# Performance work log

Hardware: AMD Instinct MI355X
Metric: run time of the kernel (lower is better)

The kernel has to match this reference:

```python
import jax, jax.numpy as jnp
import numpy as np

V = 128          # vocab_size
S = 32           # sentence_size
E = 16           # embedding_size
M = 128          # memory_size
L = 128          # linear_output_size
B = 16
N = 127


def _position_encoding(sentence_size, embedding_size):
    enc = np.ones((embedding_size, sentence_size), dtype=np.float32)
    ls = sentence_size + 1
    le = embedding_size + 1
    for i in range(1, le):
        for j in range(1, ls):
            enc[i - 1, j - 1] = (i - (le - 1) / 2) * (j - (ls - 1) / 2)
    enc = 1 + 4 * enc / embedding_size / sentence_size
    return enc.T  # [S, E]


def setup_inputs() -> dict:
    key = jax.random.key(0)
    ks = jax.random.split(key, 12)
    node_fts = jax.random.randint(ks[0], (B, N, S), 0, V).astype(jnp.float32)
    edge_fts = jax.random.randint(ks[1], (B, N, N, S), 0, V).astype(jnp.float32)
    graph_fts = jax.random.randint(ks[2], (B, S), 0, V).astype(jnp.float32)
    adj_mat = jax.random.randint(ks[3], (B, N, N), 0, 2).astype(jnp.float32)
    hidden = jnp.zeros((B, N, E), jnp.float32)
    sc = 0.02
    query_biases = sc * jax.random.normal(ks[4], (V - 1, E), jnp.float32)
    stories_biases = sc * jax.random.normal(ks[5], (V - 1, E), jnp.float32)
    output_biases = sc * jax.random.normal(ks[6], (V - 1, E), jnp.float32)
    memory_contents = sc * jax.random.normal(ks[7], (M, E), jnp.float32)
    W_int = sc * jax.random.normal(ks[8], (E, E), jnp.float32)   # intermediate_linear (unused, num_hops=1)
    W_out = sc * jax.random.normal(ks[9], (E, L), jnp.float32)   # output_linear
    W_fin = sc * jax.random.normal(ks[10], (L, V), jnp.float32)  # final_linear
    enc = jnp.asarray(_position_encoding(S, E))
    return dict(node_fts=node_fts, edge_fts=edge_fts, graph_fts=graph_fts,
                adj_mat=adj_mat, hidden=hidden, enc=enc,
                query_biases=query_biases, stories_biases=stories_biases,
                output_biases=output_biases, memory_contents=memory_contents,
                W_int=W_int, W_out=W_out, W_fin=W_fin)


def reference(node_fts, edge_fts, graph_fts, adj_mat, hidden, enc,
              query_biases, stories_biases, output_biases, memory_contents,
              W_int, W_out, W_fin):
    del hidden
    b, n, s = node_fts.shape
    # [B, N+1, S]: nodes plus graph feature row
    naf = jnp.concatenate([node_fts, graph_fts[:, None, :]], axis=1)
    # mask edges then pad to [B, N+1, N+1, S]
    ef = edge_fts * adj_mat[..., None]
    ef = jnp.pad(ef, ((0, 0), (0, 1), (0, 1), (0, 0)))
    bt = b * (n + 1)
    queries = naf.reshape(bt, s)                 # [BT, S]
    stories = ef.reshape(bt, n + 1, s)           # [BT, M0, S], M0 = N+1

    nil = jnp.zeros((1, enc.shape[1]), queries.dtype)
    sb = jnp.concatenate([stories_biases, nil], axis=0)   # [V, E]
    qb = jnp.concatenate([query_biases, nil], axis=0)
    ob = jnp.concatenate([output_biases, nil], axis=0)

    sidx = jnp.maximum(stories.astype(jnp.int32), 0)       # clamp_min(0)
    qidx = jnp.maximum(queries.astype(jnp.int32), 0)

    # position-encoded weighted sums over the sentence axis
    mem = jnp.einsum('bmse,se->bme', sb[sidx], enc)        # [BT, M0, E]
    Cj = jnp.einsum('bmse,se->bme', ob[sidx], enc)         # [BT, M0, E]
    pad_m = memory_contents.shape[0] - (n + 1)
    mem = jnp.pad(mem, ((0, 0), (0, pad_m), (0, 0))) + memory_contents
    Cj = jnp.pad(Cj, ((0, 0), (0, pad_m), (0, 0)))
    u = jnp.einsum('bse,se->be', qb[qidx], enc)            # [BT, E]

    # num_hops = 1
    x = u
    probs = jax.nn.softmax(jnp.einsum('bme,be->bm', mem, x), axis=-1)
    o = jnp.einsum('bme,bm->be', Cj, probs)
    x = jax.nn.relu((x + o) @ W_out)                       # last hop -> output_linear + relu
    ret = x @ W_fin                                        # [BT, V]

    nxt = ret.reshape(b, n + 1, -1)
    return nxt[:, :-1, :] + nxt[:, -1:, :]                 # [B, N, V]
```

## Files before the change

kernel.cpp:

```cpp
#include <hip/hip_runtime.h>

#define Vn 128
#define Sn 32
#define En 16
#define M0 128
#define Ln 128
#define Bn 16
#define Nn 127
#define NROWS (Bn * Nn)
#define RS 20

__global__ __launch_bounds__(256, 8) void memnet_fused(
    const float* __restrict__ node_fts, const float* __restrict__ edge_fts,
    const float* __restrict__ graph_fts, const float* __restrict__ adjm,
    const float* __restrict__ enc, const float* __restrict__ qb,
    const float* __restrict__ sb, const float* __restrict__ ob,
    const float* __restrict__ mc, const float* __restrict__ wout,
    const float* __restrict__ wfin, float* __restrict__ out)
{
    __shared__ __align__(16) float sbL[M0 * RS];
    __shared__ __align__(16) float encL[Sn * En];
    __shared__ unsigned int idxw[M0 * 8];
    __shared__ float scoresL[M0];
    __shared__ float probsL[M0];
    __shared__ float uL[En];
    __shared__ float ugL[En];
    __shared__ float uoL[En];
    __shared__ float cM[En];
    __shared__ float cC[En];
    __shared__ float xL[Ln];
    __shared__ float xgL[Ln];
    __shared__ float xg2L[Vn];
    __shared__ float owaveL[4 * En];
    __shared__ float red[4], red2[4];
    __shared__ int listL[128];
    __shared__ int flagL[128];
    __shared__ int wcnt[2];

    const int t = threadIdx.x;
    const int bt = blockIdx.x;
    const int b = bt / 127;
    const int lane = t & 63;
    const int wv = t >> 6;

    for (int c = t; c < 512; c += 256) {
        int r = c >> 2, q = c & 3;
        float4 v = make_float4(0.f, 0.f, 0.f, 0.f);
        if (r < 127) v = *(const float4*)&sb[r * 16 + q * 4];
        *(float4*)&sbL[r * RS + q * 4] = v;
    }
    if (t < 128) *(float4*)&encL[t * 4] = *(const float4*)&enc[t * 4];

    if (t < 128) {
        bool flag = (t < 127) && (adjm[(size_t)bt * 127 + t] != 0.f);
        unsigned long long msk = __ballot(flag);
        int pos = (int)__popcll(msk & ((1ull << lane) - 1ull));
        if (flag) listL[(t & 64) + pos] = t;
        if (lane == 0) wcnt[t >> 6] = (int)__popcll(msk);
        flagL[t] = flag ? 1 : 0;
    }
    for (int c = t; c < 1024; c += 256) {
        int m = c >> 3, q = c & 7;
        if (m < 127 && adjm[(size_t)bt * 127 + m] != 0.f) {
            float4 v = *(const float4*)&edge_fts[(size_t)(bt * 127 + m) * 32 + q * 4];
            idxw[m * 8 + q] = (unsigned)(int)v.x | ((unsigned)(int)v.y << 8)
                            | ((unsigned)(int)v.z << 16) | ((unsigned)(int)v.w << 24);
        }
    }
    if (lane < 16) {
        if (wv == 0) {
            float ue = 0.f;
            for (int s = 0; s < 32; s++) {
                int qi = (int)node_fts[(size_t)bt * 32 + s];
                if (qi < 0) qi = 0;
                float w = (qi < 127) ? qb[qi * 16 + lane] : 0.f;
                ue = fmaf(w, enc[s * 16 + lane], ue);
            }
            uL[lane] = ue;
        } else if (wv == 2) {
            float ue = 0.f;
            for (int s = 0; s < 32; s++) {
                int qi = (int)graph_fts[b * 32 + s];
                if (qi < 0) qi = 0;
                float w = (qi < 127) ? qb[qi * 16 + lane] : 0.f;
                ue = fmaf(w, enc[s * 16 + lane], ue);
            }
            ugL[lane] = ue;
        } else if (wv == 1) {
            float es = 0.f;
            for (int s = 0; s < 32; s++) es += enc[s * 16 + lane];
            cM[lane] = sb[lane] * es;
            cC[lane] = ob[lane] * es;
        }
    }
    __syncthreads();

    if (t < 128 && !flagL[t]) {
        float p = 0.f;
#pragma unroll
        for (int e4 = 0; e4 < 16; e4 += 4) {
            float4 m4 = *(const float4*)&mc[t * 16 + e4];
            p = fmaf(cM[e4 + 0] + m4.x, uL[e4 + 0], p);
            p = fmaf(cM[e4 + 1] + m4.y, uL[e4 + 1], p);
            p = fmaf(cM[e4 + 2] + m4.z, uL[e4 + 2], p);
            p = fmaf(cM[e4 + 3] + m4.w, uL[e4 + 3], p);
        }
        scoresL[t] = p;
    }

    const int eg4 = (t & 3) * 4;
    const int qd = t >> 2;
    const int c0 = wcnt[0];
    const int nact = c0 + wcnt[1];
    const float4 u4 = *(const float4*)&uL[eg4];

    float4 aC_A = make_float4(0.f, 0.f, 0.f, 0.f);
    float4 aC_B = make_float4(0.f, 0.f, 0.f, 0.f);
    int mA = -1, mB = -1;

    if (qd < nact) {
        mA = listL[(qd < c0) ? qd : (qd - c0 + 64)];
        float4 aM = make_float4(0.f, 0.f, 0.f, 0.f);
        for (int sq = 0; sq < 8; sq++) {
            unsigned w0 = idxw[mA * 8 + sq];
#pragma unroll
            for (int j = 0; j < 4; j++) {
                int s = sq * 4 + j;
                int i0 = (w0 >> (8 * j)) & 0xFF;
                int i0c = (i0 < 127) ? i0 : 126;
                float4 eb = *(const float4*)&encL[s * 16 + eg4];
                float4 a0 = *(const float4*)&sbL[i0 * RS + eg4];
                float4 cv = *(const float4*)&ob[i0c * 16 + eg4];
                if (i0 == 127) cv = make_float4(0.f, 0.f, 0.f, 0.f);
                aM.x = fmaf(a0.x, eb.x, aM.x); aM.y = fmaf(a0.y, eb.y, aM.y);
                aM.z = fmaf(a0.z, eb.z, aM.z); aM.w = fmaf(a0.w, eb.w, aM.w);
                aC_A.x = fmaf(cv.x, eb.x, aC_A.x); aC_A.y = fmaf(cv.y, eb.y, aC_A.y);
                aC_A.z = fmaf(cv.z, eb.z, aC_A.z); aC_A.w = fmaf(cv.w, eb.w, aC_A.w);
            }
        }
        float4 mc4 = *(const float4*)&mc[mA * 16 + eg4];
        float p = (aM.x + mc4.x) * u4.x + (aM.y + mc4.y) * u4.y
                + (aM.z + mc4.z) * u4.z + (aM.w + mc4.w) * u4.w;
        p += __shfl_xor(p, 1); p += __shfl_xor(p, 2);
        if ((t & 3) == 0) scoresL[mA] = p;
    }
    if (qd + 64 < nact) {
        int g = qd + 64;
        mB = listL[(g < c0) ? g : (g - c0 + 64)];
        float4 aM = make_float4(0.f, 0.f, 0.f, 0.f);
        for (int sq = 0; sq < 8; sq++) {
            unsigned w0 = idxw[mB * 8 + sq];
#pragma unroll
            for (int j = 0; j < 4; j++) {
                int s = sq * 4 + j;
                int i0 = (w0 >> (8 * j)) & 0xFF;
                int i0c = (i0 < 127) ? i0 : 126;
                float4 eb = *(const float4*)&encL[s * 16 + eg4];
                float4 a0 = *(const float4*)&sbL[i0 * RS + eg4];
                float4 cv = *(const float4*)&ob[i0c * 16 + eg4];
                if (i0 == 127) cv = make_float4(0.f, 0.f, 0.f, 0.f);
                aM.x = fmaf(a0.x, eb.x, aM.x); aM.y = fmaf(a0.y, eb.y, aM.y);
                aM.z = fmaf(a0.z, eb.z, aM.z); aM.w = fmaf(a0.w, eb.w, aM.w);
                aC_B.x = fmaf(cv.x, eb.x, aC_B.x); aC_B.y = fmaf(cv.y, eb.y, aC_B.y);
                aC_B.z = fmaf(cv.z, eb.z, aC_B.z); aC_B.w = fmaf(cv.w, eb.w, aC_B.w);
            }
        }
        float4 mc4 = *(const float4*)&mc[mB * 16 + eg4];
        float p = (aM.x + mc4.x) * u4.x + (aM.y + mc4.y) * u4.y
                + (aM.z + mc4.z) * u4.z + (aM.w + mc4.w) * u4.w;
        p += __shfl_xor(p, 1); p += __shfl_xor(p, 2);
        if ((t & 3) == 0) scoresL[mB] = p;
    }
    __syncthreads();

    float pmask;
    {
        float v = (t < 128) ? scoresL[t] : -1e30f;
#pragma unroll
        for (int off = 32; off > 0; off >>= 1) v = fmaxf(v, __shfl_xor(v, off));
        if (lane == 0) red[wv] = v;
        __syncthreads();
        float mx = fmaxf(fmaxf(red[0], red[1]), fmaxf(red[2], red[3]));
        float ex = (t < 128) ? __expf(scoresL[t] - mx) : 0.f;
        float exm = (t < 128 && !flagL[t]) ? ex : 0.f;
        float sv = ex, sm = exm;
#pragma unroll
        for (int off = 32; off > 0; off >>= 1) {
            sv += __shfl_xor(sv, off);
            sm += __shfl_xor(sm, off);
        }
        __syncthreads();
        if (lane == 0) { red[wv] = sv; red2[wv] = sm; }
        __syncthreads();
        float sum = red[0] + red[1] + red[2] + red[3];
        pmask = (red2[0] + red2[1] + red2[2] + red2[3]) / sum;
        if (t < 128) probsL[t] = ex / sum;
    }
    __syncthreads();

    {
        float4 op = make_float4(0.f, 0.f, 0.f, 0.f);
        if (mA >= 0) {
            float pa = probsL[mA];
            op.x = pa * aC_A.x; op.y = pa * aC_A.y;
            op.z = pa * aC_A.z; op.w = pa * aC_A.w;
        }
        if (mB >= 0) {
            float pb = probsL[mB];
            op.x = fmaf(pb, aC_B.x, op.x); op.y = fmaf(pb, aC_B.y, op.y);
            op.z = fmaf(pb, aC_B.z, op.z); op.w = fmaf(pb, aC_B.w, op.w);
        }
#pragma unroll
        for (int off = 4; off <= 32; off <<= 1) {
            op.x += __shfl_xor(op.x, off);
            op.y += __shfl_xor(op.y, off);
            op.z += __shfl_xor(op.z, off);
            op.w += __shfl_xor(op.w, off);
        }
        if (lane < 4) *(float4*)&owaveL[wv * 16 + lane * 4] = op;
    }
    __syncthreads();
    if (t < 16) {
        float o = owaveL[t] + owaveL[16 + t] + owaveL[32 + t] + owaveL[48 + t];
        uoL[t] = uL[t] + o + cC[t] * pmask;
    }
    __syncthreads();

    if (t < 128) {
        float acc = 0.f;
#pragma unroll
        for (int e = 0; e < 16; e++) acc = fmaf(uoL[e], wout[e * 128 + t], acc);
        xL[t] = fmaxf(acc, 0.f);
    } else {
        int l = t - 128;
        float acc = 0.f;
#pragma unroll
        for (int e = 0; e < 16; e++) acc = fmaf(ugL[e] + cC[e], wout[e * 128 + l], acc);
        xgL[l] = fmaxf(acc, 0.f);
    }
    __syncthreads();

    {
        const int vcol = t & 127;
        const float* xsrc = (t < 128) ? xL : xgL;
        float acc = 0.f;
        for (int l = 0; l < 128; l++) acc = fmaf(xsrc[l], wfin[l * 128 + vcol], acc);
        if (t >= 128) xg2L[vcol] = acc;
        __syncthreads();
        if (t < 128) out[(size_t)bt * 128 + vcol] = acc + xg2L[vcol];
    }
}

extern "C" void kernel_launch(void* const* d_in, const int* in_sizes, int n_in,
                              void* d_out, int out_size, void* d_ws, size_t ws_size,
                              hipStream_t stream)
{
    const float* node  = (const float*)d_in[0];
    const float* edge  = (const float*)d_in[1];
    const float* graph = (const float*)d_in[2];
    const float* adjm  = (const float*)d_in[3];
    const float* enc   = (const float*)d_in[5];
    const float* qb    = (const float*)d_in[6];
    const float* sb    = (const float*)d_in[7];
    const float* ob    = (const float*)d_in[8];
    const float* mc    = (const float*)d_in[9];
    const float* wout  = (const float*)d_in[11];
    const float* wfin  = (const float*)d_in[12];

    memnet_fused<<<NROWS, 256, 0, stream>>>(node, edge, graph, adjm, enc, qb,
                                            sb, ob, mc, wout, wfin, (float*)d_out);
}
```

Baseline: 132.3 us.

## Split output projection into a separate batched tail kernel sharing weights

The fused per-row kernel now stops after computing the hop output vector and writes it, plus the graph query and bias terms, to workspace. A second kernel processes 16 rows per block. It stages W_out in shared memory and uses linearity to add the graph row's activation before a single W_fin matmul, instead of doing two. This cuts the repeated per-row streaming of the 64KB W_fin and halves the final-layer FMAs. The cost is an extra kernel launch and a workspace round trip.

```diff
diff --git a/kernel.cpp b/kernel.cpp
--- a/kernel.cpp
+++ b/kernel.cpp
@@ -9,14 +9,16 @@
 #define Nn 127
 #define NROWS (Bn * Nn)
 #define RS 20
-
-__global__ __launch_bounds__(256, 8) void memnet_fused(
+#define WS_UO 0
+#define WS_UG 32768
+#define WS_CC 33024
+
+__global__ __launch_bounds__(256, 8) void memnet_core(
     const float* __restrict__ node_fts, const float* __restrict__ edge_fts,
     const float* __restrict__ graph_fts, const float* __restrict__ adjm,
     const float* __restrict__ enc, const float* __restrict__ qb,
     const float* __restrict__ sb, const float* __restrict__ ob,
-    const float* __restrict__ mc, const float* __restrict__ wout,
-    const float* __restrict__ wfin, float* __restrict__ out)
+    const float* __restrict__ mc, float* __restrict__ ws)
 {
     __shared__ __align__(16) float sbL[M0 * RS];
     __shared__ __align__(16) float encL[Sn * En];
@@ -25,12 +27,8 @@
     __shared__ float probsL[M0];
     __shared__ float uL[En];
     __shared__ float ugL[En];
-    __shared__ float uoL[En];
     __shared__ float cM[En];
     __shared__ float cC[En];
-    __shared__ float xL[Ln];
-    __shared__ float xgL[Ln];
-    __shared__ float xg2L[Vn];
     __shared__ float owaveL[4 * En];
     __shared__ float red[4], red2[4];
     __shared__ int listL[128];
@@ -222,32 +220,77 @@
     __syncthreads();
     if (t < 16) {
         float o = owaveL[t] + owaveL[16 + t] + owaveL[32 + t] + owaveL[48 + t];
-        uoL[t] = uL[t] + o + cC[t] * pmask;
-    }
-    __syncthreads();
-
+        ws[WS_UO + bt * 16 + t] = uL[t] + o + cC[t] * pmask;
+        if (bt % 127 == 0) ws[WS_UG + b * 16 + t] = ugL[t];
+        if (bt == 0) ws[WS_CC + t] = cC[t];
+    }
+}
+
+__global__ __launch_bounds__(256, 8) void memnet_tail(
+    const float* __restrict__ ws, const float* __restrict__ wout,
+    const float* __restrict__ wfin, float* __restrict__ out)
+{
+    __shared__ __align__(16) float woutL[16 * 128];
+    __shared__ float xsum[16][130];
+    __shared__ float uoT[16][16];
+    __shared__ float xgV[128];
+    __shared__ float ugcc[16];
+
+    const int t = threadIdx.x;
+    const int b = blockIdx.x >> 3;
+    const int c = blockIdx.x & 7;
+    const int i0 = c * 16;
+
+    {
+        const float4* src = (const float4*)wout;
+        float4* dst = (float4*)woutL;
+        dst[t] = src[t];
+        dst[t + 256] = src[t + 256];
+    }
+    {
+        int r = t >> 4, e = t & 15;
+        int i = i0 + r;
+        uoT[r][e] = (i < 127) ? ws[WS_UO + (size_t)(b * 127 + i) * 16 + e] : 0.f;
+        if (t < 16) ugcc[t] = ws[WS_UG + b * 16 + t] + ws[WS_CC + t];
+    }
+    __syncthreads();
     if (t < 128) {
         float acc = 0.f;
 #pragma unroll
-        for (int e = 0; e < 16; e++) acc = fmaf(uoL[e], wout[e * 128 + t], acc);
-        xL[t] = fmaxf(acc, 0.f);
-    } else {
-        int l = t - 128;
-        float acc = 0.f;
-#pragma unroll
-        for (int e = 0; e < 16; e++) acc = fmaf(ugL[e] + cC[e], wout[e * 128 + l], acc);
-        xgL[l] = fmaxf(acc, 0.f);
-    }
-    __syncthreads();
-
-    {
-        const int vcol = t & 127;
-        const float* xsrc = (t < 128) ? xL : xgL;
-        float acc = 0.f;
-        for (int l = 0; l < 128; l++) acc = fmaf(xsrc[l], wfin[l * 128 + vcol], acc);
-        if (t >= 128) xg2L[vcol] = acc;
-        __syncthreads();
-        if (t < 128) out[(size_t)bt * 128 + vcol] = acc + xg2L[vcol];
+        for (int e = 0; e < 16; e++) acc = fmaf(ugcc[e], woutL[e * 128 + t], acc);
+        xgV[t] = fmaxf(acc, 0.f);
+    }
+    __syncthreads();
+    {
+        int r = t >> 4;
+#pragma unroll
+        for (int k = 0; k < 8; k++) {
+            int l = (t & 15) + 16 * k;
+            float acc = 0.f;
+#pragma unroll
+            for (int e = 0; e < 16; e++) acc = fmaf(uoT[r][e], woutL[e * 128 + l], acc);
+            xsum[r][l] = fmaxf(acc, 0.f) + xgV[l];
+        }
+    }
+    __syncthreads();
+    {
+        int r = t >> 4, v0 = (t & 15) * 8;
+        int i = i0 + r;
+        float acc[8] = {0.f, 0.f, 0.f, 0.f, 0.f, 0.f, 0.f, 0.f};
+        for (int l = 0; l < 128; l++) {
+            float s = xsum[r][l];
+            const float4 w0 = *(const float4*)&wfin[l * 128 + v0];
+            const float4 w1 = *(const float4*)&wfin[l * 128 + v0 + 4];
+            acc[0] = fmaf(s, w0.x, acc[0]); acc[1] = fmaf(s, w0.y, acc[1]);
+            acc[2] = fmaf(s, w0.z, acc[2]); acc[3] = fmaf(s, w0.w, acc[3]);
+            acc[4] = fmaf(s, w1.x, acc[4]); acc[5] = fmaf(s, w1.y, acc[5]);
+            acc[6] = fmaf(s, w1.z, acc[6]); acc[7] = fmaf(s, w1.w, acc[7]);
+        }
+        if (i < 127) {
+            float4* o0 = (float4*)&out[((size_t)(b * 127 + i)) * 128 + v0];
+            o0[0] = make_float4(acc[0], acc[1], acc[2], acc[3]);
+            o0[1] = make_float4(acc[4], acc[5], acc[6], acc[7]);
+        }
     }
 }
 
@@ -267,6 +310,9 @@
     const float* wout  = (const float*)d_in[11];
     const float* wfin  = (const float*)d_in[12];
 
-    memnet_fused<<<NROWS, 256, 0, stream>>>(node, edge, graph, adjm, enc, qb,
-                                            sb, ob, mc, wout, wfin, (float*)d_out);
+    float* ws = (float*)d_ws;
+
+    memnet_core<<<NROWS, 256, 0, stream>>>(node, edge, graph, adjm, enc, qb,
+                                           sb, ob, mc, ws);
+    memnet_tail<<<Bn * 8, 256, 0, stream>>>(ws, wout, wfin, (float*)d_out);
 }
```

Result: slower. 136.5 us (+3.1%).
